# Kernel tuning notes

Measured on AMD Instinct MI355X. Metric: run time of the kernel, lower is better.

The kernel has to match this reference:

```python
import math
import jax, jax.numpy as jnp
import numpy as np

N_EMBD = 1024
N_HEAD = 16
B, T = 4, 2048


def _layernorm(x, g, b, eps=1e-5):
    mu = jnp.mean(x, axis=-1, keepdims=True)
    var = jnp.var(x, axis=-1, keepdims=True)
    return (x - mu) * jax.lax.rsqrt(var + eps) * g + b


def _causal_attn(x, wq, bq, wk, bk, wv, bv, wo, bo):
    Bq, Tq, C = x.shape
    H = N_HEAD
    Dh = C // H
    q = (jnp.einsum('btc,cd->btd', x, wq) + bq).reshape(Bq, Tq, H, Dh)
    k = (jnp.einsum('btc,cd->btd', x, wk) + bk).reshape(Bq, Tq, H, Dh)
    v = (jnp.einsum('btc,cd->btd', x, wv) + bv).reshape(Bq, Tq, H, Dh)
    att = jnp.einsum('bqhd,bkhd->bhqk', q, k) * (1.0 / math.sqrt(Dh))
    causal = jnp.tril(jnp.ones((Tq, Tq), dtype=bool))
    att = jnp.where(causal[None, None], att, -jnp.inf)
    att = jax.nn.softmax(att, axis=-1)
    y = jnp.einsum('bhqk,bkhd->bqhd', att, v).reshape(Bq, Tq, C)
    return jnp.einsum('btc,cd->btd', y, wo) + bo


def _mlp(x, w1, b1, w2, b2):
    h = jax.nn.gelu(jnp.einsum('btc,cf->btf', x, w1) + b1, approximate=False)
    return jnp.einsum('btf,fc->btc', h, w2) + b2


def setup_inputs() -> dict:
    key = jax.random.key(0)
    ks = jax.random.split(key, 32)
    C, F = N_EMBD, 4 * N_EMBD
    s = 0.02
    d = {'x': jax.random.normal(ks[0], (B, T, C), jnp.float32)}
    i = 1
    for a in ('a1', 'a2'):
        for n in ('wq', 'wk', 'wv', 'wo'):
            d[f'{a}_{n}'] = jax.random.normal(ks[i], (C, C), jnp.float32) * s; i += 1
            d[f'{a}_{n[1:]and "b"+n[1]}'] = jnp.zeros((C,), jnp.float32)
    for m in ('m1', 'm2'):
        d[f'{m}_w1'] = jax.random.normal(ks[i], (C, F), jnp.float32) * s; i += 1
        d[f'{m}_b1'] = jnp.zeros((F,), jnp.float32)
        d[f'{m}_w2'] = jax.random.normal(ks[i], (F, C), jnp.float32) * s; i += 1
        d[f'{m}_b2'] = jnp.zeros((C,), jnp.float32)
    for ln in ('ln1', 'ln2', 'ln3', 'ln4'):
        d[f'{ln}_g'] = jnp.ones((C,), jnp.float32)
        d[f'{ln}_b'] = jnp.zeros((C,), jnp.float32)
    # fix attention bias names: a1_bq etc.
    for a in ('a1', 'a2'):
        for hn in ('bq', 'bk', 'bv', 'bo'):
            d[f'{a}_{hn}'] = jnp.zeros((C,), jnp.float32)
    return d


def reference(x,
              a1_wq, a1_bq, a1_wk, a1_bk, a1_wv, a1_bv, a1_wo, a1_bo,
              a2_wq, a2_bq, a2_wk, a2_bk, a2_wv, a2_bv, a2_wo, a2_bo,
              m1_w1, m1_b1, m1_w2, m1_b2,
              m2_w1, m2_b1, m2_w2, m2_b2,
              ln1_g, ln1_b, ln2_g, ln2_b, ln3_g, ln3_b, ln4_g, ln4_b,
              **_ignored):
    x = x + _causal_attn(_layernorm(x, ln1_g, ln1_b),
                         a1_wq, a1_bq, a1_wk, a1_bk, a1_wv, a1_bv, a1_wo, a1_bo)
    x = x + _mlp(_layernorm(x, ln2_g, ln2_b), m1_w1, m1_b1, m1_w2, m1_b2)
    x = x + _causal_attn(_layernorm(x, ln3_g, ln3_b),
                         a2_wq, a2_bq, a2_wk, a2_bk, a2_wv, a2_bv, a2_wo, a2_bo)
    x = x + _mlp(_layernorm(x, ln4_g, ln4_b), m2_w1, m2_b1, m2_w2, m2_b2)
    return x
```

## Files before the change

### kernel.cpp

```cpp
#include <hip/hip_runtime.h>


typedef short bf16x8 __attribute__((ext_vector_type(8)));
typedef float f32x4 __attribute__((ext_vector_type(4)));

#define MFMA16(a, b, c) __builtin_amdgcn_mfma_f32_16x16x32_bf16(a, b, c, 0, 0, 0)

__device__ __forceinline__ unsigned short f2bf(float f) {
  union { float f; unsigned int u; } v; v.f = f;
  unsigned int u = v.u;
  return (unsigned short)((u + 0x7FFFu + ((u >> 16) & 1u)) >> 16);
}

__device__ __forceinline__ unsigned short f2bf_fast(float f) {
  union { float f; unsigned int u; } v; v.f = f;
  return (unsigned short)((v.u + 0x8000u) >> 16);
}

__device__ __forceinline__ float bf2f(unsigned short u) {
  union { unsigned int u; float f; } v; v.u = ((unsigned int)u) << 16;
  return v.f;
}

__device__ __forceinline__ void async16(const void* g, void* l) {
  __builtin_amdgcn_global_load_lds(
      (__attribute__((address_space(1))) void*)(g),
      (__attribute__((address_space(3))) void*)(l), 16, 0, 0);
}

__global__ __launch_bounds__(256) void transpose_cvt(
    const float* __restrict__ W, unsigned short* __restrict__ Wt, int K, int N) {
  __shared__ float t[32][33];
  int n0 = blockIdx.x * 32, k0 = blockIdx.y * 32;
  int tx = threadIdx.x, ty = threadIdx.y;
#pragma unroll
  for (int j = 0; j < 4; ++j)
    t[ty + 8 * j][tx] = W[(size_t)(k0 + ty + 8 * j) * N + n0 + tx];
  __syncthreads();
#pragma unroll
  for (int j = 0; j < 4; ++j)
    Wt[(size_t)(n0 + ty + 8 * j) * K + k0 + tx] = f2bf(t[tx][ty + 8 * j]);
}

__global__ void concat3(const float* __restrict__ a, const float* __restrict__ b,
                        const float* __restrict__ c, float* __restrict__ o) {
  int i = blockIdx.x * 256 + threadIdx.x;
  if (i < 1024) o[i] = a[i];
  else if (i < 2048) o[i] = b[i - 1024];
  else if (i < 3072) o[i] = c[i - 2048];
}

__global__ __launch_bounds__(256) void ln_kernel(
    const float* __restrict__ x, const float* __restrict__ g,
    const float* __restrict__ b, unsigned short* __restrict__ out) {
  int row = blockIdx.x;
  int tid = threadIdx.x;
  float4 v = ((const float4*)(x + (size_t)row * 1024))[tid];
  float s = v.x + v.y + v.z + v.w;
  float ss = v.x * v.x + v.y * v.y + v.z * v.z + v.w * v.w;
#pragma unroll
  for (int m = 1; m < 64; m <<= 1) {
    s += __shfl_xor(s, m);
    ss += __shfl_xor(ss, m);
  }
  __shared__ float red[8];
  int wid = tid >> 6, lane = tid & 63;
  if (lane == 0) { red[wid] = s; red[4 + wid] = ss; }
  __syncthreads();
  s = red[0] + red[1] + red[2] + red[3];
  ss = red[4] + red[5] + red[6] + red[7];
  float mean = s * (1.f / 1024.f);
  float var = ss * (1.f / 1024.f) - mean * mean;
  float rstd = rsqrtf(var + 1e-5f);
  float4 gv = ((const float4*)g)[tid];
  float4 bv = ((const float4*)b)[tid];
  ushort4 o;
  o.x = f2bf((v.x - mean) * rstd * gv.x + bv.x);
  o.y = f2bf((v.y - mean) * rstd * gv.y + bv.y);
  o.z = f2bf((v.z - mean) * rstd * gv.z + bv.z);
  o.w = f2bf((v.w - mean) * rstd * gv.w + bv.w);
  ((ushort4*)(out + (size_t)row * 1024))[tid] = o;
}

template <int MODE>
__global__ __launch_bounds__(256) void gemm_kernel(
    const unsigned short* __restrict__ A, const unsigned short* __restrict__ Bt,
    const float* __restrict__ bias, const float* resid, void* out,
    int M, int N, int K, int nbn) {
  __shared__ unsigned short As[128 * 64];
  __shared__ unsigned short Bs[128 * 64];

  int nwg = gridDim.x;
  int bid = blockIdx.x;
  int swz = (bid & 7) * (nwg >> 3) + (bid >> 3);
  int bm = swz / nbn, bn = swz % nbn;

  int tid = threadIdx.x;
  int wid = tid >> 6, lane = tid & 63;
  int wr = wid >> 1, wc = wid & 1;
  int fr = lane & 15, fg = lane >> 4;
  int srow = tid >> 3, scs = tid & 7;

  const size_t abase = (size_t)(bm * 128) * K;
  const size_t bbase = (size_t)(bn * 128) * K;

  f32x4 acc[4][4] = {};

  for (int kt = 0; kt < K; kt += 64) {
    __syncthreads();
#pragma unroll
    for (int i = 0; i < 4; ++i) {
      int row = i * 32 + srow;
      int c = scs ^ (row & 7);
      async16(A + abase + (size_t)row * K + kt + 8 * c, As + i * 2048 + wid * 512);
    }
#pragma unroll
    for (int i = 0; i < 4; ++i) {
      int row = i * 32 + srow;
      int c = scs ^ (row & 7);
      async16(Bt + bbase + (size_t)row * K + kt + 8 * c, Bs + i * 2048 + wid * 512);
    }
    __syncthreads();
#pragma unroll
    for (int ks = 0; ks < 2; ++ks) {
      bf16x8 af[4], bf[4];
#pragma unroll
      for (int f = 0; f < 4; ++f) {
        int ra = wr * 64 + f * 16 + fr;
        int ca = (ks * 4 + fg) ^ (ra & 7);
        af[f] = *(const bf16x8*)(As + ra * 64 + ca * 8);
        int rb = wc * 64 + f * 16 + fr;
        int cb = (ks * 4 + fg) ^ (rb & 7);
        bf[f] = *(const bf16x8*)(Bs + rb * 64 + cb * 8);
      }
#pragma unroll
      for (int a = 0; a < 4; ++a)
#pragma unroll
        for (int b2 = 0; b2 < 4; ++b2)
          acc[a][b2] = MFMA16(af[a], bf[b2], acc[a][b2]);
    }
  }

  int m0 = bm * 128 + wr * 64, n0 = bn * 128 + wc * 64;
#pragma unroll
  for (int a = 0; a < 4; ++a) {
#pragma unroll
    for (int b2 = 0; b2 < 4; ++b2) {
      int n = n0 + b2 * 16 + fr;
      float bsv = bias[n];
#pragma unroll
      for (int r = 0; r < 4; ++r) {
        int m = m0 + a * 16 + fg * 4 + r;
        float v = acc[a][b2][r] + bsv;
        if (MODE == 0) {
          ((unsigned short*)out)[(size_t)m * N + n] = f2bf(v);
        } else if (MODE == 1) {
          v = 0.5f * v * (1.0f + erff(v * 0.70710678118654752f));
          ((unsigned short*)out)[(size_t)m * N + n] = f2bf(v);
        } else {
          ((float*)out)[(size_t)m * N + n] = resid[(size_t)m * N + n] + v;
        }
      }
    }
  }
}

__global__ __launch_bounds__(256) void attn_kernel(
    const unsigned short* __restrict__ qkv, unsigned short* __restrict__ y) {
  __shared__ unsigned short Ks[64 * 64];
  __shared__ unsigned short Vt[64 * 72];
  __shared__ unsigned short Pf[4][16 * 72];

  int qt = 31 - (int)blockIdx.x;
  int bh = blockIdx.y;
  int b = bh >> 4, h = bh & 15;
  int tid = threadIdx.x, wid = tid >> 6, lane = tid & 63;
  int fr = lane & 15, fg = lane >> 4;

  const unsigned short* qp = qkv + (size_t)(b * 2048) * 3072 + h * 64;
  const unsigned short* kp = qp + 1024;
  const unsigned short* vp = qp + 2048;

  int qrow = qt * 64 + wid * 16 + fr;
  const unsigned short* qrp = qp + (size_t)qrow * 3072;
  bf16x8 qf[2];
#pragma unroll
  for (int ks = 0; ks < 2; ++ks) {
    bf16x8 raw = *(const bf16x8*)(qrp + ks * 32 + 8 * fg);
#pragma unroll
    for (int j = 0; j < 8; ++j)
      qf[ks][j] = (short)f2bf(bf2f((unsigned short)raw[j]) * 0.125f);
  }

  float rs[4] = {0.f, 0.f, 0.f, 0.f};
  f32x4 oacc[4] = {};

  int kvp = tid & 31, dgrp = tid >> 5;
  int srow8 = tid >> 3, scs = tid & 7;

  for (int t = 0; t <= qt; ++t) {
    int kv0 = t * 64;
    __syncthreads();
#pragma unroll
    for (int i = 0; i < 2; ++i) {
      int row = i * 32 + srow8;
      int c = scs ^ (row & 7);
      async16(kp + (size_t)(kv0 + row) * 3072 + 8 * c, Ks + i * 2048 + wid * 512);
    }
    {
      const unsigned short* v0 = vp + (size_t)(kv0 + 2 * kvp) * 3072 + 8 * dgrp;
      bf16x8 ra = *(const bf16x8*)v0;
      bf16x8 rb = *(const bf16x8*)(v0 + 3072);
      unsigned int* base = (unsigned int*)Vt;
#pragma unroll
      for (int j = 0; j < 8; ++j)
        base[(8 * dgrp + j) * 36 + kvp] =
            (unsigned int)(unsigned short)ra[j] |
            ((unsigned int)(unsigned short)rb[j] << 16);
    }
    __syncthreads();

    f32x4 s[4];
#pragma unroll
    for (int n = 0; n < 4; ++n) {
      s[n] = (f32x4){0.f, 0.f, 0.f, 0.f};
#pragma unroll
      for (int ks = 0; ks < 2; ++ks) {
        int row = n * 16 + fr;
        int cs = (ks * 4 + fg) ^ (row & 7);
        bf16x8 kf = *(const bf16x8*)(Ks + row * 64 + cs * 8);
        s[n] = MFMA16(qf[ks], kf, s[n]);
      }
    }

    if (t == qt) {
      int qb = qt * 64 + wid * 16 + fg * 4;
#pragma unroll
      for (int n = 0; n < 4; ++n)
#pragma unroll
        for (int r = 0; r < 4; ++r)
          if (kv0 + n * 16 + fr > qb + r) s[n][r] = -1e30f;
    }

    unsigned short* pw = Pf[wid];
#pragma unroll
    for (int n = 0; n < 4; ++n)
#pragma unroll
      for (int r = 0; r < 4; ++r) {
        float p = __expf(s[n][r]);
        rs[r] += p;
        pw[(fg * 4 + r) * 72 + n * 16 + fr] = f2bf_fast(p);
      }

    bf16x8 pa[2];
    pa[0] = *(const bf16x8*)(pw + fr * 72 + 8 * fg);
    pa[1] = *(const bf16x8*)(pw + fr * 72 + 32 + 8 * fg);

#pragma unroll
    for (int d = 0; d < 4; ++d)
#pragma unroll
      for (int ks = 0; ks < 2; ++ks) {
        bf16x8 vf = *(const bf16x8*)(Vt + (d * 16 + fr) * 72 + ks * 32 + 8 * fg);
        oacc[d] = MFMA16(pa[ks], vf, oacc[d]);
      }
  }

#pragma unroll
  for (int m2 = 1; m2 < 16; m2 <<= 1)
#pragma unroll
    for (int r = 0; r < 4; ++r) rs[r] += __shfl_xor(rs[r], m2);

  unsigned short* yp = y + (size_t)(b * 2048 + qt * 64 + wid * 16) * 1024 + h * 64;
#pragma unroll
  for (int d = 0; d < 4; ++d)
#pragma unroll
    for (int r = 0; r < 4; ++r) {
      float val = oacc[d][r] / rs[r];
      yp[(size_t)(fg * 4 + r) * 1024 + d * 16 + fr] = f2bf(val);
    }
}

extern "C" void kernel_launch(void* const* d_in, const int* in_sizes, int n_in,
                              void* d_out, int out_size, void* d_ws, size_t ws_size,
                              hipStream_t stream) {
  (void)in_sizes; (void)n_in; (void)out_size; (void)ws_size;
  char* ws = (char*)d_ws;
  unsigned short* ACT1 = (unsigned short*)(ws);
  unsigned short* ACT2 = (unsigned short*)(ws + 16777216);
  unsigned short* WQKV1 = (unsigned short*)(ws + 83886080);
  unsigned short* WO1   = (unsigned short*)(ws + 90177536);
  unsigned short* WQKV2 = (unsigned short*)(ws + 92274688);
  unsigned short* WO2   = (unsigned short*)(ws + 98566144);
  unsigned short* WF1_1 = (unsigned short*)(ws + 100663296);
  unsigned short* WF2_1 = (unsigned short*)(ws + 109051904);
  unsigned short* WF1_2 = (unsigned short*)(ws + 117440512);
  unsigned short* WF2_2 = (unsigned short*)(ws + 125829120);
  float* BQKV1 = (float*)(ws + 134217728);
  float* BQKV2 = (float*)(ws + 134230016);

  const float* x = (const float*)d_in[0];
  float* OUT = (float*)d_out;

  auto T = [&](int idx, unsigned short* dst, int K, int N) {
    transpose_cvt<<<dim3(N / 32, K / 32), dim3(32, 8), 0, stream>>>(
        (const float*)d_in[idx], dst, K, N);
  };
  T(1, WQKV1, 1024, 1024); T(3, WQKV1 + 1024 * 1024, 1024, 1024);
  T(5, WQKV1 + 2 * 1024 * 1024, 1024, 1024); T(7, WO1, 1024, 1024);
  T(9, WQKV2, 1024, 1024); T(11, WQKV2 + 1024 * 1024, 1024, 1024);
  T(13, WQKV2 + 2 * 1024 * 1024, 1024, 1024); T(15, WO2, 1024, 1024);
  T(17, WF1_1, 1024, 4096); T(19, WF2_1, 4096, 1024);
  T(21, WF1_2, 1024, 4096); T(23, WF2_2, 4096, 1024);
  concat3<<<12, 256, 0, stream>>>((const float*)d_in[2], (const float*)d_in[4],
                                  (const float*)d_in[6], BQKV1);
  concat3<<<12, 256, 0, stream>>>((const float*)d_in[10], (const float*)d_in[12],
                                  (const float*)d_in[14], BQKV2);

  auto LN = [&](const float* in, int gi, int bi) {
    ln_kernel<<<8192, 256, 0, stream>>>(in, (const float*)d_in[gi],
                                        (const float*)d_in[bi], ACT1);
  };
  auto G = [&](int mode, const unsigned short* A, const unsigned short* Bt,
               const float* bias, const float* resid, void* out, int N, int K) {
    int nbn = N / 128;
    int nwg = 64 * nbn;
    if (mode == 0)
      gemm_kernel<0><<<nwg, 256, 0, stream>>>(A, Bt, bias, resid, out, 8192, N, K, nbn);
    else if (mode == 1)
      gemm_kernel<1><<<nwg, 256, 0, stream>>>(A, Bt, bias, resid, out, 8192, N, K, nbn);
    else
      gemm_kernel<2><<<nwg, 256, 0, stream>>>(A, Bt, bias, resid, out, 8192, N, K, nbn);
  };

  LN(x, 25, 26);
  G(0, ACT1, WQKV1, BQKV1, nullptr, ACT2, 3072, 1024);
  attn_kernel<<<dim3(32, 64), 256, 0, stream>>>(ACT2, ACT1);
  G(2, ACT1, WO1, (const float*)d_in[8], x, OUT, 1024, 1024);
  LN(OUT, 27, 28);
  G(1, ACT1, WF1_1, (const float*)d_in[18], nullptr, ACT2, 4096, 1024);
  G(2, ACT2, WF2_1, (const float*)d_in[20], OUT, OUT, 1024, 4096);
  LN(OUT, 29, 30);
  G(0, ACT1, WQKV2, BQKV2, nullptr, ACT2, 3072, 1024);
  attn_kernel<<<dim3(32, 64), 256, 0, stream>>>(ACT2, ACT1);
  G(2, ACT1, WO2, (const float*)d_in[16], OUT, OUT, 1024, 1024);
  LN(OUT, 31, 32);
  G(1, ACT1, WF1_2, (const float*)d_in[22], nullptr, ACT2, 4096, 1024);
  G(2, ACT2, WF2_2, (const float*)d_in[24], OUT, OUT, 1024, 4096);
}
```

Baseline: 1.139 ms.

## Add 256x256 double-buffered GEMM and pipeline attention K/V loads

Adds a 512-thread GEMM with a 256x256 tile, double-buffered async LDS staging and MFMA priority raising, and uses it for the QKV and FC1 projections. Restructures attention to double-buffer K in LDS, prefetch V into registers one tile ahead, transpose the QK product so each lane keeps a single row sum, and pack P writes as 32-bit words. The goal is to hide global load latency and raise data reuse per tile. In exchange, shared memory and register use per block go up, and the larger GEMM tile produces fewer workgroups per launch.

New measurement: 1.125 ms. No clear change (-1.3%).

```diff
diff --git a/kernel.cpp b/kernel.cpp
--- a/kernel.cpp
+++ b/kernel.cpp
@@ -3,8 +3,10 @@
 
 typedef short bf16x8 __attribute__((ext_vector_type(8)));
 typedef float f32x4 __attribute__((ext_vector_type(4)));
+typedef unsigned int u32;
 
 #define MFMA16(a, b, c) __builtin_amdgcn_mfma_f32_16x16x32_bf16(a, b, c, 0, 0, 0)
+#define SCHED_FENCE() __builtin_amdgcn_sched_barrier(0)
 
 __device__ __forceinline__ unsigned short f2bf(float f) {
   union { float f; unsigned int u; } v; v.f = f;
@@ -165,11 +167,118 @@
   }
 }
 
+template <int MODE>
+__global__ __launch_bounds__(512, 2) void gemm256(
+    const unsigned short* __restrict__ A, const unsigned short* __restrict__ Bt,
+    const float* __restrict__ bias, const float* resid, void* out,
+    int M, int N, int K, int nbn) {
+  __shared__ unsigned short As[2][256 * 64];
+  __shared__ unsigned short Bs[2][256 * 64];
+
+  int nwg = gridDim.x;
+  int bid = blockIdx.x;
+  int swz = (bid & 7) * (nwg >> 3) + (bid >> 3);
+  int bm = swz / nbn, bn = swz % nbn;
+
+  int tid = threadIdx.x;
+  int wid = tid >> 6, lane = tid & 63;
+  int wm = wid >> 2, wn = wid & 3;
+  int fr = lane & 15, fg = lane >> 4;
+  int srow = tid >> 3, su = tid & 7;
+  int sc = su ^ (srow & 7);
+
+  const size_t abase = (size_t)(bm * 256) * K;
+  const size_t bbase = (size_t)(bn * 256) * K;
+
+  f32x4 acc[8][4] = {};
+
+  auto STAGE = [&](int pp, int kt) {
+#pragma unroll
+    for (int i = 0; i < 4; ++i)
+      async16(A + abase + (size_t)(i * 64 + srow) * K + kt + sc * 8,
+              &As[pp][i * 4096 + tid * 8]);
+#pragma unroll
+    for (int i = 0; i < 4; ++i)
+      async16(Bt + bbase + (size_t)(i * 64 + srow) * K + kt + sc * 8,
+              &Bs[pp][i * 4096 + tid * 8]);
+  };
+
+  const int NT = K >> 6;
+  STAGE(0, 0);
+
+  for (int kt = 0; kt < NT; ++kt) {
+    int p = kt & 1;
+    if (kt + 1 < NT) {
+      STAGE(p ^ 1, (kt + 1) * 64);
+      asm volatile("s_waitcnt vmcnt(8)" ::: "memory");
+    } else {
+      asm volatile("s_waitcnt vmcnt(0)" ::: "memory");
+    }
+    SCHED_FENCE();
+    __builtin_amdgcn_s_barrier();
+    SCHED_FENCE();
+
+    bf16x8 bfr[4][2];
+#pragma unroll
+    for (int n = 0; n < 4; ++n)
+#pragma unroll
+      for (int ks = 0; ks < 2; ++ks)
+        bfr[n][ks] = *(const bf16x8*)(
+            &Bs[p][(wn * 64 + n * 16 + fr) * 64 + ((ks * 4 + fg) ^ (fr & 7)) * 8]);
+#pragma unroll
+    for (int qm = 0; qm < 2; ++qm) {
+      bf16x8 afr[4][2];
+#pragma unroll
+      for (int a = 0; a < 4; ++a)
+#pragma unroll
+        for (int ks = 0; ks < 2; ++ks)
+          afr[a][ks] = *(const bf16x8*)(
+              &As[p][(wm * 128 + qm * 64 + a * 16 + fr) * 64 + ((ks * 4 + fg) ^ (fr & 7)) * 8]);
+      __builtin_amdgcn_s_setprio(1);
+#pragma unroll
+      for (int ks = 0; ks < 2; ++ks)
+#pragma unroll
+        for (int a = 0; a < 4; ++a)
+#pragma unroll
+          for (int n = 0; n < 4; ++n)
+            acc[qm * 4 + a][n] = MFMA16(afr[a][ks], bfr[n][ks], acc[qm * 4 + a][n]);
+      __builtin_amdgcn_s_setprio(0);
+    }
+
+    SCHED_FENCE();
+    __builtin_amdgcn_s_barrier();
+    SCHED_FENCE();
+  }
+
+  int m0 = bm * 256 + wm * 128, n0 = bn * 256 + wn * 64;
+#pragma unroll
+  for (int a = 0; a < 8; ++a) {
+#pragma unroll
+    for (int n = 0; n < 4; ++n) {
+      int col = n0 + n * 16 + fr;
+      float bsv = bias[col];
+#pragma unroll
+      for (int r = 0; r < 4; ++r) {
+        int row = m0 + a * 16 + fg * 4 + r;
+        float v = acc[a][n][r] + bsv;
+        if (MODE == 0) {
+          ((unsigned short*)out)[(size_t)row * N + col] = f2bf(v);
+        } else if (MODE == 1) {
+          v = 0.5f * v * (1.0f + erff(v * 0.70710678118654752f));
+          ((unsigned short*)out)[(size_t)row * N + col] = f2bf(v);
+        } else {
+          ((float*)out)[(size_t)row * N + col] = resid[(size_t)row * N + col] + v;
+        }
+      }
+    }
+  }
+}
+
 __global__ __launch_bounds__(256) void attn_kernel(
     const unsigned short* __restrict__ qkv, unsigned short* __restrict__ y) {
-  __shared__ unsigned short Ks[64 * 64];
-  __shared__ unsigned short Vt[64 * 72];
-  __shared__ unsigned short Pf[4][16 * 72];
+  __shared__ unsigned short Ks[2][64 * 64];
+  __shared__ unsigned short Vt[2][64 * 72];
+  __shared__ u32 Pf[4][16 * 36];
 
   int qt = 31 - (int)blockIdx.x;
   int bh = blockIdx.y;
@@ -192,35 +301,48 @@
       qf[ks][j] = (short)f2bf(bf2f((unsigned short)raw[j]) * 0.125f);
   }
 
-  float rs[4] = {0.f, 0.f, 0.f, 0.f};
+  float rs = 0.f;
   f32x4 oacc[4] = {};
 
   int kvp = tid & 31, dgrp = tid >> 5;
-  int srow8 = tid >> 3, scs = tid & 7;
+
+  auto stageK = [&](int t, int p) {
+#pragma unroll
+    for (int i = 0; i < 2; ++i) {
+      int row = i * 32 + (tid >> 3);
+      int c = (tid & 7) ^ (row & 7);
+      async16(kp + (size_t)(t * 64 + row) * 3072 + 8 * c, &Ks[p][i * 2048 + tid * 8]);
+    }
+  };
+  bf16x8 rva, rvb;
+  auto loadV = [&](int t) {
+    const unsigned short* v0 = vp + (size_t)(t * 64 + 2 * kvp) * 3072 + 8 * dgrp;
+    rva = *(const bf16x8*)v0;
+    rvb = *(const bf16x8*)(v0 + 3072);
+  };
+
+  stageK(0, 0);
+  loadV(0);
 
   for (int t = 0; t <= qt; ++t) {
-    int kv0 = t * 64;
-    __syncthreads();
-#pragma unroll
-    for (int i = 0; i < 2; ++i) {
-      int row = i * 32 + srow8;
-      int c = scs ^ (row & 7);
-      async16(kp + (size_t)(kv0 + row) * 3072 + 8 * c, Ks + i * 2048 + wid * 512);
-    }
+    int p = t & 1;
+    if (t < qt) stageK(t + 1, p ^ 1);
     {
-      const unsigned short* v0 = vp + (size_t)(kv0 + 2 * kvp) * 3072 + 8 * dgrp;
-      bf16x8 ra = *(const bf16x8*)v0;
-      bf16x8 rb = *(const bf16x8*)(v0 + 3072);
-      unsigned int* base = (unsigned int*)Vt;
+      u32* base = (u32*)Vt[p];
 #pragma unroll
       for (int j = 0; j < 8; ++j)
         base[(8 * dgrp + j) * 36 + kvp] =
-            (unsigned int)(unsigned short)ra[j] |
-            ((unsigned int)(unsigned short)rb[j] << 16);
-    }
-    __syncthreads();
+            (u32)(unsigned short)rva[j] | ((u32)(unsigned short)rvb[j] << 16);
+    }
+    asm volatile("s_waitcnt vmcnt(4)" ::: "memory");
+    asm volatile("s_waitcnt lgkmcnt(0)" ::: "memory");
+    SCHED_FENCE();
+    __builtin_amdgcn_s_barrier();
+    SCHED_FENCE();
+    if (t < qt) loadV(t + 1);
 
     f32x4 s[4];
+    __builtin_amdgcn_s_setprio(1);
 #pragma unroll
     for (int n = 0; n < 4; ++n) {
       s[n] = (f32x4){0.f, 0.f, 0.f, 0.f};
@@ -228,56 +350,61 @@
       for (int ks = 0; ks < 2; ++ks) {
         int row = n * 16 + fr;
         int cs = (ks * 4 + fg) ^ (row & 7);
-        bf16x8 kf = *(const bf16x8*)(Ks + row * 64 + cs * 8);
-        s[n] = MFMA16(qf[ks], kf, s[n]);
+        bf16x8 kf = *(const bf16x8*)(&Ks[p][row * 64 + cs * 8]);
+        s[n] = MFMA16(kf, qf[ks], s[n]);
       }
     }
+    __builtin_amdgcn_s_setprio(0);
 
     if (t == qt) {
-      int qb = qt * 64 + wid * 16 + fg * 4;
 #pragma unroll
       for (int n = 0; n < 4; ++n)
 #pragma unroll
         for (int r = 0; r < 4; ++r)
-          if (kv0 + n * 16 + fr > qb + r) s[n][r] = -1e30f;
-    }
-
-    unsigned short* pw = Pf[wid];
-#pragma unroll
-    for (int n = 0; n < 4; ++n)
-#pragma unroll
-      for (int r = 0; r < 4; ++r) {
-        float p = __expf(s[n][r]);
-        rs[r] += p;
-        pw[(fg * 4 + r) * 72 + n * 16 + fr] = f2bf_fast(p);
+          if (n * 16 + fg * 4 + r > wid * 16 + fr) s[n][r] = -1e30f;
+    }
+
+    u32* Pw = Pf[wid];
+#pragma unroll
+    for (int n = 0; n < 4; ++n) {
+      float p0 = __expf(s[n][0]), p1 = __expf(s[n][1]);
+      float p2 = __expf(s[n][2]), p3 = __expf(s[n][3]);
+      rs += (p0 + p1) + (p2 + p3);
+      Pw[fr * 36 + 8 * n + 2 * fg + 0] = (u32)f2bf_fast(p0) | ((u32)f2bf_fast(p1) << 16);
+      Pw[fr * 36 + 8 * n + 2 * fg + 1] = (u32)f2bf_fast(p2) | ((u32)f2bf_fast(p3) << 16);
+    }
+
+    bf16x8 pa[2];
+    pa[0] = *(const bf16x8*)(Pw + fr * 36 + 0 * 16 + fg * 4);
+    pa[1] = *(const bf16x8*)(Pw + fr * 36 + 1 * 16 + fg * 4);
+
+    __builtin_amdgcn_s_setprio(1);
+#pragma unroll
+    for (int db = 0; db < 4; ++db)
+#pragma unroll
+      for (int ks = 0; ks < 2; ++ks) {
+        bf16x8 vf = *(const bf16x8*)(&Vt[p][(db * 16 + fr) * 72 + ks * 32 + 8 * fg]);
+        oacc[db] = MFMA16(pa[ks], vf, oacc[db]);
       }
-
-    bf16x8 pa[2];
-    pa[0] = *(const bf16x8*)(pw + fr * 72 + 8 * fg);
-    pa[1] = *(const bf16x8*)(pw + fr * 72 + 32 + 8 * fg);
-
-#pragma unroll
-    for (int d = 0; d < 4; ++d)
-#pragma unroll
-      for (int ks = 0; ks < 2; ++ks) {
-        bf16x8 vf = *(const bf16x8*)(Vt + (d * 16 + fr) * 72 + ks * 32 + 8 * fg);
-        oacc[d] = MFMA16(pa[ks], vf, oacc[d]);
-      }
-  }
-
-#pragma unroll
-  for (int m2 = 1; m2 < 16; m2 <<= 1)
-#pragma unroll
-    for (int r = 0; r < 4; ++r) rs[r] += __shfl_xor(rs[r], m2);
-
+    __builtin_amdgcn_s_setprio(0);
+
+    SCHED_FENCE();
+    __builtin_amdgcn_s_barrier();
+    SCHED_FENCE();
+  }
+
+  float rt = rs;
+  rt += __shfl_xor(rt, 16);
+  rt += __shfl_xor(rt, 32);
   unsigned short* yp = y + (size_t)(b * 2048 + qt * 64 + wid * 16) * 1024 + h * 64;
 #pragma unroll
-  for (int d = 0; d < 4; ++d)
-#pragma unroll
-    for (int r = 0; r < 4; ++r) {
-      float val = oacc[d][r] / rs[r];
-      yp[(size_t)(fg * 4 + r) * 1024 + d * 16 + fr] = f2bf(val);
-    }
+  for (int r = 0; r < 4; ++r) {
+    float dn = __shfl(rt, fg * 4 + r);
+    float inv = 1.0f / dn;
+#pragma unroll
+    for (int db = 0; db < 4; ++db)
+      yp[(size_t)(fg * 4 + r) * 1024 + db * 16 + fr] = f2bf(oacc[db][r] * inv);
+  }
 }
 
 extern "C" void kernel_launch(void* const* d_in, const int* in_sizes, int n_in,
@@ -331,19 +458,30 @@
     else
       gemm_kernel<2><<<nwg, 256, 0, stream>>>(A, Bt, bias, resid, out, 8192, N, K, nbn);
   };
+  auto G256 = [&](int mode, const unsigned short* A, const unsigned short* Bt,
+                  const float* bias, const float* resid, void* out, int N, int K) {
+    int nbn = N / 256;
+    int nwg = 32 * nbn;
+    if (mode == 0)
+      gemm256<0><<<nwg, 512, 0, stream>>>(A, Bt, bias, resid, out, 8192, N, K, nbn);
+    else if (mode == 1)
+      gemm256<1><<<nwg, 512, 0, stream>>>(A, Bt, bias, resid, out, 8192, N, K, nbn);
+    else
+      gemm256<2><<<nwg, 512, 0, stream>>>(A, Bt, bias, resid, out, 8192, N, K, nbn);
+  };
 
   LN(x, 25, 26);
-  G(0, ACT1, WQKV1, BQKV1, nullptr, ACT2, 3072, 1024);
+  G256(0, ACT1, WQKV1, BQKV1, nullptr, ACT2, 3072, 1024);
   attn_kernel<<<dim3(32, 64), 256, 0, stream>>>(ACT2, ACT1);
   G(2, ACT1, WO1, (const float*)d_in[8], x, OUT, 1024, 1024);
   LN(OUT, 27, 28);
-  G(1, ACT1, WF1_1, (const float*)d_in[18], nullptr, ACT2, 4096, 1024);
+  G256(1, ACT1, WF1_1, (const float*)d_in[18], nullptr, ACT2, 4096, 1024);
   G(2, ACT2, WF2_1, (const float*)d_in[20], OUT, OUT, 1024, 4096);
   LN(OUT, 29, 30);
-  G(0, ACT1, WQKV2, BQKV2, nullptr, ACT2, 3072, 1024);
+  G256(0, ACT1, WQKV2, BQKV2, nullptr, ACT2, 3072, 1024);
   attn_kernel<<<dim3(32, 64), 256, 0, stream>>>(ACT2, ACT1);
   G(2, ACT1, WO2, (const float*)d_in[16], OUT, OUT, 1024, 1024);
   LN(OUT, 31, 32);
-  G(1, ACT1, WF1_2, (const float*)d_in[22], nullptr, ACT2, 4096, 1024);
+  G256(1, ACT1, WF1_2, (const float*)d_in[22], nullptr, ACT2, 4096, 1024);
   G(2, ACT2, WF2_2, (const float*)d_in[24], OUT, OUT, 1024, 4096);
 }
```
